# Optimization experiments

Measured on AMD Instinct MI355X. Metric: run time of the kernel, lower is better.

## Reference

```python
import jax, jax.numpy as jnp
import numpy as np


def conv1d_same(x, w, b):
    # x:[B,C,W], w:[O,I,K] -> [B,O,W] (stride 1, SAME padding, k=11,p=5)
    y = jax.lax.conv_general_dilated(x, w, (1,), 'SAME',
                                     dimension_numbers=('NCH', 'OIH', 'NCH'))
    return y + b[None, :, None]


def maxpool8(x):
    B, C, W = x.shape
    return x.reshape(B, C, W // 8, 8).max(axis=-1)


def encoder(x, p):
    back1 = jax.nn.relu(conv1d_same(x, p['e_c1_w'], p['e_c1_b']))   # [B,64,1280]
    h = maxpool8(back1)                                              # [B,64,160]
    back2 = jax.nn.relu(conv1d_same(h, p['e_c2_w'], p['e_c2_b']))   # [B,128,160]
    h = maxpool8(back2)                                              # [B,128,20]
    h = h.reshape(h.shape[0], -1)                                    # [B,2560]
    h = jax.nn.relu(h @ p['e_f1_w'].T + p['e_f1_b'])
    fea = jax.nn.sigmoid(h @ p['e_f2_w'].T + p['e_f2_b'])            # [B,64]
    return back1, back2, fea


def decoder(fea, back1, back2, p):
    h = jax.nn.relu(fea @ p['d_f1_w'].T + p['d_f1_b'])
    h = jax.nn.relu(h @ p['d_f2_w'].T + p['d_f2_b'])                 # [B,2560]
    h = h.reshape(h.shape[0], 128, 20)
    h = jnp.repeat(h, 8, axis=-1)                                    # nearest upsample -> 160
    h = jax.nn.relu(conv1d_same(jnp.concatenate([h, back2], 1), p['d_c2_w'], p['d_c2_b']))
    h = jnp.repeat(h, 8, axis=-1)                                    # -> 1280
    h = jax.nn.relu(conv1d_same(jnp.concatenate([h, back1], 1), p['d_c1_w'], p['d_c1_b']))
    return h                                                         # [B,2,1280]


def pairwise_kl(fea_s, fea_t, lab_s, lab_t, L):
    # Group rows by label. jnp.argsort is stable, so within each label the
    # original row order is preserved, exactly like torch boolean-mask gather.
    # Equal per-label counts are assumed (required by F.kl_div shape match).
    gs = fea_s[jnp.argsort(lab_s)].reshape(L, -1, fea_s.shape[-1])
    gt = fea_t[jnp.argsort(lab_t)].reshape(L, -1, fea_t.shape[-1])
    T = jnp.concatenate([gs, gt], axis=1)          # [L, M, D]
    logT = jnp.log(T)
    M = T.shape[1] * T.shape[2]
    # kl_div(t_i.log(), t_j) with reduction='mean' = mean(t_j*(log t_j - log t_i))
    A = jnp.sum(T * logT, axis=(1, 2)) / M         # [L]: mean(t_j log t_j)
    C = jnp.einsum('imd,jmd->ij', logT, T) / M     # C[i,j] = mean(t_j log t_i)
    kl = (L - 1) * A.sum() - (C.sum() - jnp.trace(C))  # sum over i != j
    return (kl / (L * L / 2.0))[None]              # shape [1] like torch.zeros(1)


def setup_inputs() -> dict:
    key = jax.random.key(0)
    ks = jax.random.split(key, 12)
    B, L, W = 256, 8, 1280

    def w(k, shape, fan_in):
        return (jax.random.normal(k, shape, jnp.float32) / np.sqrt(fan_in)).astype(jnp.float32)

    return {
        'x_source': jax.random.normal(ks[0], (B, 2, W), jnp.float32),
        'x_target': jax.random.normal(ks[1], (B, 2, W), jnp.float32),
        'x_s_label': jnp.arange(B, dtype=jnp.int32) % L,  # balanced labels
        'x_t_label': jnp.arange(B, dtype=jnp.int32) % L,
        'label_all': L,
        'e_c1_w': w(ks[2], (64, 2, 11), 2 * 11),    'e_c1_b': jnp.zeros(64, jnp.float32),
        'e_c2_w': w(ks[3], (128, 64, 11), 64 * 11), 'e_c2_b': jnp.zeros(128, jnp.float32),
        'e_f1_w': w(ks[4], (512, 2560), 2560),      'e_f1_b': jnp.zeros(512, jnp.float32),
        'e_f2_w': w(ks[5], (64, 512), 512),         'e_f2_b': jnp.zeros(64, jnp.float32),
        'd_f1_w': w(ks[6], (256, 64), 64),          'd_f1_b': jnp.zeros(256, jnp.float32),
        'd_f2_w': w(ks[7], (2560, 256), 256),       'd_f2_b': jnp.zeros(2560, jnp.float32),
        'd_c2_w': w(ks[8], (64, 256, 11), 256 * 11),'d_c2_b': jnp.zeros(64, jnp.float32),
        'd_c1_w': w(ks[9], (2, 128, 11), 128 * 11), 'd_c1_b': jnp.zeros(2, jnp.float32),
    }


def reference(x_source, x_target, x_s_label, x_t_label, label_all,
              e_c1_w, e_c1_b, e_c2_w, e_c2_b, e_f1_w, e_f1_b, e_f2_w, e_f2_b,
              d_f1_w, d_f1_b, d_f2_w, d_f2_b, d_c2_w, d_c2_b, d_c1_w, d_c1_b):
    p = {'e_c1_w': e_c1_w, 'e_c1_b': e_c1_b, 'e_c2_w': e_c2_w, 'e_c2_b': e_c2_b,
         'e_f1_w': e_f1_w, 'e_f1_b': e_f1_b, 'e_f2_w': e_f2_w, 'e_f2_b': e_f2_b,
         'd_f1_w': d_f1_w, 'd_f1_b': d_f1_b, 'd_f2_w': d_f2_w, 'd_f2_b': d_f2_b,
         'd_c2_w': d_c2_w, 'd_c2_b': d_c2_b, 'd_c1_w': d_c1_w, 'd_c1_b': d_c1_b}
    back1_s, back2_s, fea_s = encoder(x_source, p)
    back1_t, back2_t, fea_t = encoder(x_target, p)
    out_s = decoder(fea_s, back1_t, back2_t, p)
    out_t = decoder(fea_t, back1_s, back2_s, p)
    kl = pairwise_kl(fea_s, fea_t, x_s_label, x_t_label, label_all)
    return out_s, out_t, kl
```

## Files before the change

### kernel.cpp

```cpp
#include <hip/hip_runtime.h>
#include <hip/hip_bf16.h>
#include <math.h>

#define BB   256
#define LLc  8
#define DDc  64
#define GSc  32

typedef __attribute__((ext_vector_type(8))) short short8;
typedef __attribute__((ext_vector_type(4))) float f32x4;
typedef unsigned short u16;

__device__ inline float b2f(u16 h) { return __uint_as_float(((unsigned)h) << 16); }
__device__ inline u16 f2b(float f) {
  unsigned u = __float_as_uint(f);
  return (u16)((u + 0x7fffu + ((u >> 16) & 1u)) >> 16);
}

#define PRE_W2P   90112
#define PRE_WD2P  270336
#define PRE_WD1P  292864
#define PRE_EF1   1603584
#define PRE_DF2   2258944
#define PRE_UPT   2521088
#define PRE_B2T   3569664
#define PRE_W1P   3571712
#define PRE_B1T   4096000
#define PRE_D2T   4161536
__global__ __launch_bounds__(256) void prep_k(const float* __restrict__ ec2w, const float* __restrict__ dc2w,
                       const float* __restrict__ dc1w, const float* __restrict__ ef1w,
                       const float* __restrict__ df2w, const float* __restrict__ ec1w,
                       u16* __restrict__ W2p, u16* __restrict__ Wd2p, u16* __restrict__ Wd1p,
                       u16* __restrict__ ef1wbf, u16* __restrict__ df2wbf, u16* __restrict__ W1p,
                       u16* __restrict__ upT_s, u16* __restrict__ upT_t,
                       u16* __restrict__ b2T_s, u16* __restrict__ b2T_t,
                       u16* __restrict__ b1T_s, u16* __restrict__ b1T_t,
                       u16* __restrict__ d2T_s, u16* __restrict__ d2T_t) {
  int idx = blockIdx.x * 256 + threadIdx.x;
  if (idx < PRE_W2P) {
    int k = idx / 8192, oc = (idx / 64) % 128, ic = idx % 64;
    W2p[idx] = f2b(ec2w[(oc * 64 + ic) * 11 + k]);
  } else if (idx < PRE_WD2P) {
    int j = idx - PRE_W2P;
    int k = j / 16384, oc = (j / 256) % 64, icc = j % 256;
    Wd2p[j] = f2b(dc2w[(oc * 256 + icc) * 11 + k]);
  } else if (idx < PRE_WD1P) {
    int j = idx - PRE_WD2P;
    int k = j / 2048, rem = j % 2048;
    int chunk = rem / 512, oc = (rem / 32) % 16, c = rem % 32;
    Wd1p[j] = (oc < 2) ? f2b(dc1w[((size_t)oc * 128 + chunk * 32 + c) * 11 + k]) : 0;
  } else if (idx < PRE_EF1) {
    int j = idx - PRE_WD1P;
    ef1wbf[j] = f2b(ef1w[j]);
  } else if (idx < PRE_DF2) {
    int j = idx - PRE_EF1;
    df2wbf[j] = f2b(df2w[j]);
  } else if (idx < PRE_UPT) {
    int j = idx - PRE_DF2;
    int ic = j % 128, r4 = (j / 128) % 4, b = (j / 512) % 256, side = j / 131072;
    int row = (r4 == 0) ? 0 : (20 + r4);
    (side ? upT_t : upT_s)[((size_t)b * 24 + row) * 128 + ic] = 0;
  } else if (idx < PRE_B2T) {
    int j = idx - PRE_UPT;
    int ic = j % 128, pr = (j / 128) % 16, b = (j / 2048) % 256, side = j / 524288;
    int row = (pr < 8) ? pr : pr + 160;
    (side ? b2T_t : b2T_s)[((size_t)b * 176 + row) * 128 + ic] = 0;
  } else if (idx < PRE_W1P) {
    int j = idx - PRE_B2T;
    int oc = j >> 5, kk = j & 31, ic = kk >> 4, k = kk & 15;
    W1p[j] = (k < 11) ? f2b(ec1w[oc * 22 + ic * 11 + k]) : 0;
  } else if (idx < PRE_B1T) {
    int j = idx - PRE_W1P;
    int ic = j % 64, pr = (j / 64) % 16, b = (j / 1024) % 256, side = j / 262144;
    int row = (pr < 5) ? pr : 1280 + pr;
    (side ? b1T_t : b1T_s)[((size_t)b * 1296 + row) * 64 + ic] = 0;
  } else if (idx < PRE_D2T) {
    int j = idx - PRE_B1T;
    int ic = j % 64, pr = (j / 64) & 1, b = (j / 128) % 256, side = j / 32768;
    int row = pr ? 161 : 0;
    (side ? d2T_t : d2T_s)[((size_t)b * 162 + row) * 64 + ic] = 0;
  }
}

__global__ __launch_bounds__(256) void im2col1_k(const float* __restrict__ x_s, const float* __restrict__ x_t,
                          u16* __restrict__ xcol_s, u16* __restrict__ xcol_t) {
  int bk = blockIdx.x;
  int side = bk >= 320;
  int idx = (bk - (side ? 320 : 0)) * 256 + threadIdx.x;
  int wg = idx % 160, ic = (idx / 160) & 1, b = idx / 320;
  int w0 = wg * 8;
  const float* xb = (side ? x_t : x_s) + (size_t)(b * 2 + ic) * 1280;
  u16* xcol = side ? xcol_t : xcol_s;
  u16 win[18];
#pragma unroll
  for (int j = 0; j < 18; j++) {
    int p = w0 - 5 + j;
    win[j] = (p >= 0 && p < 1280) ? f2b(xb[p]) : 0;
  }
#pragma unroll
  for (int r = 0; r < 8; r++) {
    uint4 s0, s1;
    s0.x = (unsigned)win[r + 0] | ((unsigned)win[r + 1] << 16);
    s0.y = (unsigned)win[r + 2] | ((unsigned)win[r + 3] << 16);
    s0.z = (unsigned)win[r + 4] | ((unsigned)win[r + 5] << 16);
    s0.w = (unsigned)win[r + 6] | ((unsigned)win[r + 7] << 16);
    s1.x = (unsigned)win[r + 8] | ((unsigned)win[r + 9] << 16);
    s1.y = (unsigned)win[r + 10];
    s1.z = 0; s1.w = 0;
    u16* dst = xcol + ((size_t)(b * 1280 + w0 + r) * 32 + ic * 16);
    *(uint4*)dst = s0;
    *(uint4*)(dst + 8) = s1;
  }
}

__global__ __launch_bounds__(256) void conv1_mfma(const u16* __restrict__ xcol_s, const u16* __restrict__ xcol_t,
                           const u16* __restrict__ W1p, const float* __restrict__ bias,
                           u16* __restrict__ b1T_s, u16* __restrict__ b1T_t) {
  int blk = blockIdx.x;
  int side = blk >> 10;
  int r = blk & 1023;
  int b = r >> 2, wq = r & 3;
  const u16* xcol = side ? xcol_t : xcol_s;
  u16* back1T = side ? b1T_t : b1T_s;
  int tid = threadIdx.x, wid = tid >> 6, l = tid & 63;
  int l15 = l & 15, lq = l >> 4;
  int oc0 = wid * 16;
  int w0 = wq * 320;
  short8 a = *(const short8*)(W1p + (oc0 + l15) * 32 + lq * 8);
  f32x4 zero = {0.f, 0.f, 0.f, 0.f};
  f32x4 acc[20];
#pragma unroll
  for (int j = 0; j < 20; j++) acc[j] = zero;
  const u16* xb = xcol + (size_t)b * 1280 * 32;
#pragma unroll
  for (int nf = 0; nf < 20; nf++) {
    int w = w0 + nf * 16 + l15;
    short8 bf = *(const short8*)(xb + (size_t)w * 32 + lq * 8);
    acc[nf] = __builtin_amdgcn_mfma_f32_16x16x32_bf16(a, bf, acc[nf], 0, 0, 0);
  }
  int ocb = oc0 + lq * 4;
  float b0 = bias[ocb], b1 = bias[ocb + 1], b2 = bias[ocb + 2], b3 = bias[ocb + 3];
#pragma unroll
  for (int nf = 0; nf < 20; nf++) {
    int w = w0 + nf * 16 + l15;
    uint2 st;
    st.x = (unsigned)f2b(fmaxf(acc[nf][0] + b0, 0.f)) | ((unsigned)f2b(fmaxf(acc[nf][1] + b1, 0.f)) << 16);
    st.y = (unsigned)f2b(fmaxf(acc[nf][2] + b2, 0.f)) | ((unsigned)f2b(fmaxf(acc[nf][3] + b3, 0.f)) << 16);
    *(uint2*)(back1T + ((size_t)b * 1296 + w + 5) * 64 + ocb) = st;
  }
}

__global__ __launch_bounds__(256) void pool1T_k(const u16* __restrict__ b1T_s, const u16* __restrict__ b1T_t,
                         u16* __restrict__ p1T_s, u16* __restrict__ p1T_t) {
  int bk = blockIdx.x;
  int side = bk >= 11264;
  int idx = (bk - (side ? 11264 : 0)) * 256 + threadIdx.x;
  int ic = idx % 64, row = (idx / 64) % 176, b = idx / 11264;
  const u16* back1T = side ? b1T_t : b1T_s;
  u16 val = 0;
  if (row >= 8 && row < 168) {
    const u16* pp = back1T + ((size_t)b * 1296 + (row - 8) * 8 + 5) * 64 + ic;
    float m = b2f(pp[0]);
#pragma unroll
    for (int j = 1; j < 8; j++) m = fmaxf(m, b2f(pp[j * 64]));
    val = f2b(m);
  }
  (side ? p1T_t : p1T_s)[idx] = val;
}

__global__ __launch_bounds__(256) void conv2_split(const u16* __restrict__ p1T_s, const u16* __restrict__ p1T_t,
                            const u16* __restrict__ W2p, const float* __restrict__ bias,
                            u16* __restrict__ b2T_s, u16* __restrict__ b2T_t) {
  __shared__ u16 smem[90 * 72];
  int blk = blockIdx.x;
  int side = blk >> 10;
  int r = blk & 1023;
  int b = r >> 2, wh = (r >> 1) & 1, oh = r & 1;
  const u16* p1T = side ? p1T_t : p1T_s;
  u16* back2T = side ? b2T_t : b2T_s;
  int tid = threadIdx.x, wid = tid >> 6, l = tid & 63;
  int l15 = l & 15, lq = l >> 4;
  int oc0 = oh * 64 + wid * 16;
  int w0 = wh * 80;
  const u16* pb = p1T + (size_t)b * 176 * 64;
  for (int i = tid; i < 720; i += 256) {
    int row = i >> 3, seg = i & 7;
    *(uint4*)(&smem[row * 72 + seg * 8]) = *(const uint4*)(pb + ((size_t)(w0 + 3 + row)) * 64 + seg * 8);
  }
  __syncthreads();
  f32x4 zero = {0.f, 0.f, 0.f, 0.f};
  f32x4 acc[5];
#pragma unroll
  for (int j = 0; j < 5; j++) acc[j] = zero;
  for (int k = 0; k < 11; k++) {
    for (int ic0 = 0; ic0 < 64; ic0 += 32) {
      short8 a = *(const short8*)(W2p + ((k * 128 + oc0 + l15) * 64 + ic0 + lq * 8));
      short8 bf[5];
#pragma unroll
      for (int nf = 0; nf < 5; nf++)
        bf[nf] = *(const short8*)(&smem[(nf * 16 + l15 + k) * 72 + ic0 + lq * 8]);
#pragma unroll
      for (int nf = 0; nf < 5; nf++)
        acc[nf] = __builtin_amdgcn_mfma_f32_16x16x32_bf16(a, bf[nf], acc[nf], 0, 0, 0);
    }
  }
  int ocb = oc0 + lq * 4;
  float b0 = bias[ocb], b1 = bias[ocb + 1], b2 = bias[ocb + 2], b3 = bias[ocb + 3];
#pragma unroll
  for (int nf = 0; nf < 5; nf++) {
    int w = w0 + nf * 16 + l15;
    f32x4 v = acc[nf];
    uint2 st;
    st.x = (unsigned)f2b(fmaxf(v[0] + b0, 0.f)) | ((unsigned)f2b(fmaxf(v[1] + b1, 0.f)) << 16);
    st.y = (unsigned)f2b(fmaxf(v[2] + b2, 0.f)) | ((unsigned)f2b(fmaxf(v[3] + b3, 0.f)) << 16);
    *(uint2*)(back2T + ((size_t)(b * 176 + 8 + w) * 128 + ocb)) = st;
  }
}

__global__ __launch_bounds__(256) void pool2_k(const u16* __restrict__ b2T_s, const u16* __restrict__ b2T_t,
                        u16* __restrict__ p2bf_s, u16* __restrict__ p2bf_t) {
  int bk = blockIdx.x;
  int side = bk >= 2560;
  int idx = (bk - (side ? 2560 : 0)) * 256 + threadIdx.x;
  int wo = idx % 20, oc = (idx / 20) % 128, b = idx / 2560;
  const u16* b2T = side ? b2T_t : b2T_s;
  float m = -1e30f;
#pragma unroll
  for (int j = 0; j < 8; j++)
    m = fmaxf(m, b2f(b2T[((size_t)b * 176 + 8 + wo * 8 + j) * 128 + oc]));
  (side ? p2bf_t : p2bf_s)[idx] = f2b(m);
}

__global__ __launch_bounds__(256) void ef1_split(const u16* __restrict__ A_s, const u16* __restrict__ A_t,
                          const u16* __restrict__ Bw, float* __restrict__ pbuf) {
  int blk = blockIdx.x;
  int side = blk >> 8;
  int r = blk & 255;
  int kc = r >> 5;
  int q = r & 31;
  int n0 = (q & 7) * 64;
  int tid = threadIdx.x, wid = tid >> 6, l = tid & 63;
  int l15 = l & 15, lq = l >> 4;
  int m0 = (q >> 3) * 64 + wid * 16;
  const u16* A = side ? A_t : A_s;
  f32x4 zero = {0.f, 0.f, 0.f, 0.f};
  f32x4 acc[4];
#pragma unroll
  for (int j = 0; j < 4; j++) acc[j] = zero;
  int kbase = kc * 320;
  for (int k0 = kbase; k0 < kbase + 320; k0 += 32) {
    short8 af = *(const short8*)(A + ((size_t)(m0 + l15) * 2560 + k0 + lq * 8));
    short8 bf[4];
#pragma unroll
    for (int nf = 0; nf < 4; nf++)
      bf[nf] = *(const short8*)(Bw + ((size_t)(n0 + nf * 16 + l15) * 2560 + k0 + lq * 8));
#pragma unroll
    for (int nf = 0; nf < 4; nf++)
      acc[nf] = __builtin_amdgcn_mfma_f32_16x16x32_bf16(af, bf[nf], acc[nf], 0, 0, 0);
  }
  int bb = m0 + lq * 4;
  float* pb = pbuf + (size_t)(side * 8 + kc) * 131072;
#pragma unroll
  for (int nf = 0; nf < 4; nf++) {
    int oc = n0 + nf * 16 + l15;
#pragma unroll
    for (int rr = 0; rr < 4; rr++)
      pb[(size_t)(bb + rr) * 512 + oc] = acc[nf][rr];
  }
}

__global__ __launch_bounds__(256) void ef1_red(const float* __restrict__ pbuf, const float* __restrict__ bias,
                        float* __restrict__ ef1_s, float* __restrict__ ef1_t) {
  int e = blockIdx.x * 256 + threadIdx.x;
  int side = e >> 17;
  int j = e & 131071;
  const float* pb = pbuf + (size_t)side * 8 * 131072;
  float s = 0.f;
#pragma unroll
  for (int kc = 0; kc < 8; kc++) s += pb[(size_t)kc * 131072 + j];
  s += bias[j & 511];
  (side ? ef1_t : ef1_s)[j] = fmaxf(s, 0.f);
}

__global__ __launch_bounds__(256) void ef2df1_k(const float* __restrict__ ef1_s, const float* __restrict__ ef1_t,
                         const float* __restrict__ ef2w, const float* __restrict__ ef2b,
                         const float* __restrict__ df1w, const float* __restrict__ df1b,
                         float* __restrict__ fea_s, float* __restrict__ fea_t,
                         u16* __restrict__ df1bf_s, u16* __restrict__ df1bf_t) {
  __shared__ float row[512];
  __shared__ float part[256];
  __shared__ float fea_sh[64];
  int side = blockIdx.x >> 8;
  int b = blockIdx.x & 255;
  const float* ef1 = side ? ef1_t : ef1_s;
  float* fea = side ? fea_t : fea_s;
  u16* df1bf = side ? df1bf_t : df1bf_s;
  int tid = threadIdx.x;
  row[tid] = ef1[(size_t)b * 512 + tid];
  row[tid + 256] = ef1[(size_t)b * 512 + tid + 256];
  __syncthreads();
  {
    int o = tid & 63, q = tid >> 6;
    const float4* wr = (const float4*)(ef2w + (size_t)o * 512 + q * 128);
    float s = 0.f;
    int base = q * 128;
#pragma unroll
    for (int i = 0; i < 32; i++) {
      float4 wv = wr[i];
      s += row[base + 4 * i] * wv.x + row[base + 4 * i + 1] * wv.y +
           row[base + 4 * i + 2] * wv.z + row[base + 4 * i + 3] * wv.w;
    }
    part[q * 64 + o] = s;
  }
  __syncthreads();
  if (tid < 64) {
    float v = part[tid] + part[64 + tid] + part[128 + tid] + part[192 + tid] + ef2b[tid];
    float sg = 1.f / (1.f + expf(-v));
    fea_sh[tid] = sg;
    fea[(size_t)b * 64 + tid] = sg;
  }
  __syncthreads();
  {
    const float4* wr = (const float4*)(df1w + (size_t)tid * 64);
    float s = 0.f;
#pragma unroll
    for (int i = 0; i < 16; i++) {
      float4 wv = wr[i];
      s += fea_sh[4 * i] * wv.x + fea_sh[4 * i + 1] * wv.y +
           fea_sh[4 * i + 2] * wv.z + fea_sh[4 * i + 3] * wv.w;
    }
    df1bf[(size_t)b * 256 + tid] = f2b(fmaxf(s + df1b[tid], 0.f));
  }
}

__global__ __launch_bounds__(256) void df2_gemm(const u16* __restrict__ A_s, const u16* __restrict__ A_t,
                         const u16* __restrict__ Bw, const float* __restrict__ bias,
                         u16* __restrict__ upT_s, u16* __restrict__ upT_t) {
  int blk = blockIdx.x;
  int side = blk >= 40;
  int n0 = (blk - (side ? 40 : 0)) * 64;
  const u16* A = side ? A_t : A_s;
  u16* upT = side ? upT_t : upT_s;
  int tid = threadIdx.x, wid = tid >> 6, l = tid & 63;
  int l15 = l & 15, lq = l >> 4;
  int m0 = wid * 64;
  f32x4 zero = {0.f, 0.f, 0.f, 0.f};
  f32x4 acc[4][4];
#pragma unroll
  for (int i = 0; i < 4; i++)
#pragma unroll
    for (int j = 0; j < 4; j++) acc[i][j] = zero;
  for (int k0 = 0; k0 < 256; k0 += 32) {
    short8 af[4], bf[4];
#pragma unroll
    for (int mf = 0; mf < 4; mf++)
      af[mf] = *(const short8*)(A + ((size_t)(m0 + mf * 16 + l15) * 256 + k0 + lq * 8));
#pragma unroll
    for (int nf = 0; nf < 4; nf++)
      bf[nf] = *(const short8*)(Bw + ((size_t)(n0 + nf * 16 + l15) * 256 + k0 + lq * 8));
#pragma unroll
    for (int mf = 0; mf < 4; mf++)
#pragma unroll
      for (int nf = 0; nf < 4; nf++)
        acc[mf][nf] = __builtin_amdgcn_mfma_f32_16x16x32_bf16(af[mf], bf[nf], acc[mf][nf], 0, 0, 0);
  }
#pragma unroll
  for (int nf = 0; nf < 4; nf++) {
    int o = n0 + nf * 16 + l15;
    float bi = bias[o];
    int ch = o / 20, t = o - ch * 20;
#pragma unroll
    for (int mf = 0; mf < 4; mf++) {
      int bb = m0 + mf * 16 + lq * 4;
#pragma unroll
      for (int r = 0; r < 4; r++)
        upT[((size_t)(bb + r) * 24 + 1 + t) * 128 + ch] = f2b(fmaxf(acc[mf][nf][r] + bi, 0.f));
    }
  }
}

__global__ __launch_bounds__(256) void convd2_split(const u16* __restrict__ upT_s, const u16* __restrict__ upT_t,
                             const u16* __restrict__ b2T_s, const u16* __restrict__ b2T_t,
                             const u16* __restrict__ Wd2p, float* __restrict__ part) {
  __shared__ u16 smem[90 * 136];
  int blk = blockIdx.x;
  int side = blk >> 10;
  int r = blk & 1023;
  int b = r >> 2, wh = (r >> 1) & 1, khalf = r & 1;
  const u16* upT   = side ? upT_t : upT_s;
  const u16* skipT = side ? b2T_s : b2T_t;
  int tid = threadIdx.x, wid = tid >> 6, l = tid & 63;
  int l15 = l & 15, lq = l >> 4;
  int oc0 = wid * 16;
  int w0 = wh * 80;
  const u16* sb = skipT + (size_t)b * 176 * 128;
  for (int i = tid; i < 1440; i += 256) {
    int row = i >> 4, seg = i & 15;
    *(uint4*)(&smem[row * 136 + seg * 8]) = *(const uint4*)(sb + ((size_t)(w0 + 3 + row)) * 128 + seg * 8);
  }
  __syncthreads();
  f32x4 zero = {0.f, 0.f, 0.f, 0.f};
  f32x4 acc[5];
#pragma unroll
  for (int j = 0; j < 5; j++) acc[j] = zero;
  const u16* ub = upT + (size_t)b * 24 * 128;
  int kbeg = khalf ? 6 : 0, kend = khalf ? 11 : 6;
  for (int k = kbeg; k < kend; k++) {
    for (int ic0 = 0; ic0 < 128; ic0 += 32) {
      short8 a = *(const short8*)(Wd2p + ((k * 64 + oc0 + l15) * 256 + ic0 + lq * 8));
#pragma unroll
      for (int nf = 0; nf < 5; nf++) {
        int w = w0 + nf * 16 + l15;
        int rr = (w + k + 3) >> 3;
        short8 bf = *(const short8*)(ub + (rr * 128 + ic0 + lq * 8));
        acc[nf] = __builtin_amdgcn_mfma_f32_16x16x32_bf16(a, bf, acc[nf], 0, 0, 0);
      }
    }
    for (int ic0 = 0; ic0 < 128; ic0 += 32) {
      short8 a = *(const short8*)(Wd2p + ((k * 64 + oc0 + l15) * 256 + 128 + ic0 + lq * 8));
#pragma unroll
      for (int nf = 0; nf < 5; nf++) {
        short8 bf = *(const short8*)(&smem[(nf * 16 + l15 + k) * 136 + ic0 + lq * 8]);
        acc[nf] = __builtin_amdgcn_mfma_f32_16x16x32_bf16(a, bf, acc[nf], 0, 0, 0);
      }
    }
  }
  float* pp = part + (((size_t)(side * 2 + khalf) * 256 + b) * 160) * 64;
  int ocb = oc0 + lq * 4;
#pragma unroll
  for (int nf = 0; nf < 5; nf++) {
    int w = w0 + nf * 16 + l15;
    *(f32x4*)(pp + (size_t)w * 64 + ocb) = acc[nf];
  }
}

__global__ __launch_bounds__(256) void convd2_red(const float* __restrict__ part, const float* __restrict__ bias,
                           u16* __restrict__ d2T_s, u16* __restrict__ d2T_t) {
  int idx = blockIdx.x * 256 + threadIdx.x;
  int oc4 = (idx & 15) * 4;
  int w = (idx >> 4) % 160;
  int rb = (idx >> 4) / 160;
  int b = rb & 255;
  int side = rb >> 8;
  const float* p0 = part + (((size_t)(side * 2 + 0) * 256 + b) * 160 + w) * 64 + oc4;
  const float* p1 = part + (((size_t)(side * 2 + 1) * 256 + b) * 160 + w) * 64 + oc4;
  float4 a = *(const float4*)p0;
  float4 c = *(const float4*)p1;
  float b0 = bias[oc4], b1 = bias[oc4 + 1], b2 = bias[oc4 + 2], b3 = bias[oc4 + 3];
  uint2 st;
  st.x = (unsigned)f2b(fmaxf(a.x + c.x + b0, 0.f)) | ((unsigned)f2b(fmaxf(a.y + c.y + b1, 0.f)) << 16);
  st.y = (unsigned)f2b(fmaxf(a.z + c.z + b2, 0.f)) | ((unsigned)f2b(fmaxf(a.w + c.w + b3, 0.f)) << 16);
  u16* dst = side ? d2T_t : d2T_s;
  *(uint2*)(dst + ((size_t)b * 162 + w + 1) * 64 + oc4) = st;
}

__global__ __launch_bounds__(256) void convd1_mfma(const u16* __restrict__ d2T_s, const u16* __restrict__ d2T_t,
                            const u16* __restrict__ b1T_s, const u16* __restrict__ b1T_t,
                            const u16* __restrict__ Wd1p, const float* __restrict__ bias,
                            float* __restrict__ out_s, float* __restrict__ out_t) {
  __shared__ u16 smem[330 * 72];
  int blk = blockIdx.x;
  int side = blk >> 10;
  int r = blk & 1023;
  int b = r >> 2, q = r & 3;
  const u16* dc2T   = side ? d2T_t : d2T_s;
  const u16* back1T = side ? b1T_s : b1T_t;
  float* out = side ? out_t : out_s;
  int tid = threadIdx.x, wid = tid >> 6, l = tid & 63;
  int l15 = l & 15, lq = l >> 4;
  int base = q * 320;
  int wloc0 = wid * 80;
  const u16* sb = back1T + (size_t)b * 1296 * 64;
  for (int i = tid; i < 2640; i += 256) {
    int row = i >> 3, seg = i & 7;
    *(uint4*)(&smem[row * 72 + seg * 8]) = *(const uint4*)(sb + ((size_t)(base + row)) * 64 + seg * 8);
  }
  __syncthreads();
  f32x4 zero = {0.f, 0.f, 0.f, 0.f};
  f32x4 acc[5];
#pragma unroll
  for (int j = 0; j < 5; j++) acc[j] = zero;
  const u16* ub = dc2T + (size_t)b * 162 * 64;
  for (int k = 0; k < 11; k++) {
#pragma unroll
    for (int ch = 0; ch < 2; ch++) {
      short8 wf = *(const short8*)(Wd1p + ((k * 4 + ch) * 16 + l15) * 32 + lq * 8);
#pragma unroll
      for (int nf = 0; nf < 5; nf++) {
        int w = base + wloc0 + nf * 16 + l15;
        int rr = (w + k + 3) >> 3;
        short8 af = *(const short8*)(ub + (rr * 64 + ch * 32 + lq * 8));
        acc[nf] = __builtin_amdgcn_mfma_f32_16x16x32_bf16(af, wf, acc[nf], 0, 0, 0);
      }
    }
#pragma unroll
    for (int ch = 0; ch < 2; ch++) {
      short8 wf = *(const short8*)(Wd1p + ((k * 4 + 2 + ch) * 16 + l15) * 32 + lq * 8);
#pragma unroll
      for (int nf = 0; nf < 5; nf++) {
        int lrow = wloc0 + nf * 16 + l15 + k;
        short8 af = *(const short8*)(&smem[lrow * 72 + ch * 32 + lq * 8]);
        acc[nf] = __builtin_amdgcn_mfma_f32_16x16x32_bf16(af, wf, acc[nf], 0, 0, 0);
      }
    }
  }
  if (l15 < 2) {
    float bi = bias[l15];
    float* ob = out + ((size_t)b * 2 + l15) * 1280;
#pragma unroll
    for (int nf = 0; nf < 5; nf++) {
      int wbase = base + wloc0 + nf * 16 + lq * 4;
      float4 v;
      v.x = fmaxf(acc[nf][0] + bi, 0.f);
      v.y = fmaxf(acc[nf][1] + bi, 0.f);
      v.z = fmaxf(acc[nf][2] + bi, 0.f);
      v.w = fmaxf(acc[nf][3] + bi, 0.f);
      *(float4*)(ob + wbase) = v;
    }
  }
}

__global__ void kl_sort_k(const int* __restrict__ lab_s, const int* __restrict__ lab_t,
                          int* __restrict__ srt) {
  int t = threadIdx.x;
  {
    int lab = lab_s[t];
    int pos = 0;
    for (int b = 0; b < BB; b++) {
      int lb = lab_s[b];
      pos += (lb < lab) + ((b < t) && (lb == lab));
    }
    srt[pos] = t;
  }
  {
    int lab = lab_t[t];
    int pos = 0;
    for (int b = 0; b < BB; b++) {
      int lb = lab_t[b];
      pos += (lb < lab) + ((b < t) && (lb == lab));
    }
    srt[256 + pos] = t;
  }
}

__global__ void kl_build_k(const float* __restrict__ fea_s, const float* __restrict__ fea_t,
                           const int* __restrict__ srt,
                           float* __restrict__ T, float* __restrict__ logT) {
  int idx = blockIdx.x * 256 + threadIdx.x;
#pragma unroll
  for (int r = 0; r < 4; r++) {
    int e = idx + r * 8192;
    int d = e & 63;
    int m = (e >> 6) & 63;
    int l = e >> 12;
    float v;
    if (m < GSc) v = fea_s[srt[l * GSc + m] * DDc + d];
    else         v = fea_t[srt[256 + l * GSc + (m - GSc)] * DDc + d];
    T[e]    = v;
    logT[e] = logf(v);
  }
}

__global__ void kl_pairs_k(const float* __restrict__ T, const float* __restrict__ logT,
                           float* __restrict__ C) {
  int blk = blockIdx.x;
  int i = blk >> 3, j = blk & 7;
  int t = threadIdx.x;
  __shared__ float wsum[4];
  const float* li = logT + i * 4096;
  const float* tj = T + j * 4096;
  float s = 0.f;
  for (int e = t; e < 4096; e += 256) s += li[e] * tj[e];
  for (int off = 32; off > 0; off >>= 1) s += __shfl_down(s, off, 64);
  if ((t & 63) == 0) wsum[t >> 6] = s;
  __syncthreads();
  if (t == 0) C[blk] = wsum[0] + wsum[1] + wsum[2] + wsum[3];
}

__global__ void kl_final_k(const float* __restrict__ C, float* __restrict__ out) {
  int t = threadIdx.x;
  float c = C[t];
  float tr = ((t >> 3) == (t & 7)) ? c : 0.f;
  for (int off = 32; off > 0; off >>= 1) {
    c  += __shfl_down(c, off, 64);
    tr += __shfl_down(tr, off, 64);
  }
  if (t == 0) out[0] = (LLc * tr - c) / 4096.f / (LLc * LLc / 2.0f);
}

extern "C" void kernel_launch(void* const* d_in, const int* in_sizes, int n_in,
                              void* d_out, int out_size, void* d_ws, size_t ws_size,
                              hipStream_t stream) {
  const float* x_s  = (const float*)d_in[0];
  const float* x_t  = (const float*)d_in[1];
  const int* lab_s  = (const int*)d_in[2];
  const int* lab_t  = (const int*)d_in[3];
  const float* ec1w = (const float*)d_in[5];  const float* ec1b = (const float*)d_in[6];
  const float* ec2w = (const float*)d_in[7];  const float* ec2b = (const float*)d_in[8];
  const float* ef1w = (const float*)d_in[9];  const float* ef1b = (const float*)d_in[10];
  const float* ef2w = (const float*)d_in[11]; const float* ef2b = (const float*)d_in[12];
  const float* df1w = (const float*)d_in[13]; const float* df1b = (const float*)d_in[14];
  const float* df2w = (const float*)d_in[15]; const float* df2b = (const float*)d_in[16];
  const float* dc2w = (const float*)d_in[17]; const float* dc2b = (const float*)d_in[18];
  const float* dc1w = (const float*)d_in[19]; const float* dc1b = (const float*)d_in[20];

  char* p = (char*)d_ws;
  auto alloc = [&](size_t bytes) -> char* {
    char* r = p;
    p += (bytes + 255) & ~(size_t)255;
    return r;
  };
  u16*   b1T_s   = (u16*)alloc((size_t)BB * 1296 * 64 * 2);
  u16*   b1T_t   = (u16*)alloc((size_t)BB * 1296 * 64 * 2);
  u16*   xcol_s  = (u16*)alloc((size_t)BB * 1280 * 32 * 2);
  u16*   xcol_t  = (u16*)alloc((size_t)BB * 1280 * 32 * 2);
  u16*   p1T_s   = (u16*)alloc((size_t)BB * 176 * 64 * 2);
  u16*   p1T_t   = (u16*)alloc((size_t)BB * 176 * 64 * 2);
  u16*   b2T_s   = (u16*)alloc((size_t)BB * 176 * 128 * 2);
  u16*   b2T_t   = (u16*)alloc((size_t)BB * 176 * 128 * 2);
  u16*   upT_s   = (u16*)alloc((size_t)BB * 24 * 128 * 2);
  u16*   upT_t   = (u16*)alloc((size_t)BB * 24 * 128 * 2);
  u16*   p2bf_s  = (u16*)alloc((size_t)BB * 2560 * 2);
  u16*   p2bf_t  = (u16*)alloc((size_t)BB * 2560 * 2);
  float* ef1_s   = (float*)alloc((size_t)BB * 512 * 4);
  float* ef1_t   = (float*)alloc((size_t)BB * 512 * 4);
  float* fea_s   = (float*)alloc((size_t)BB * 64 * 4);
  float* fea_t   = (float*)alloc((size_t)BB * 64 * 4);
  u16*   df1bf_s = (u16*)alloc((size_t)BB * 256 * 2);
  u16*   df1bf_t = (u16*)alloc((size_t)BB * 256 * 2);
  u16*   d2T_s   = (u16*)alloc((size_t)BB * 162 * 64 * 2);
  u16*   d2T_t   = (u16*)alloc((size_t)BB * 162 * 64 * 2);
  u16*   W2p     = (u16*)alloc(90112 * 2);
  u16*   Wd2p    = (u16*)alloc(180224 * 2);
  u16*   Wd1p    = (u16*)alloc(22528 * 2);
  u16*   ef1wbf  = (u16*)alloc((size_t)1310720 * 2);
  u16*   df2wbf  = (u16*)alloc((size_t)655360 * 2);
  u16*   W1p     = (u16*)alloc(2048 * 2);
  float* Tbuf    = (float*)alloc((size_t)32768 * 4);
  float* logTbuf = (float*)alloc((size_t)32768 * 4);
  int*   srt     = (int*)alloc(512 * 4);
  float* Cbuf    = (float*)alloc(64 * 4);
  float* pbuf    = (float*)xcol_s;
  float* part    = (float*)xcol_t;

  float* out_s  = (float*)d_out;
  float* out_t  = out_s + (size_t)BB * 2 * 1280;
  float* out_kl = out_s + (size_t)2 * BB * 2 * 1280;

  dim3 blk(256);

  prep_k<<<dim3(16256), blk, 0, stream>>>(ec2w, dc2w, dc1w, ef1w, df2w, ec1w,
                                          W2p, Wd2p, Wd1p, ef1wbf, df2wbf, W1p,
                                          upT_s, upT_t, b2T_s, b2T_t,
                                          b1T_s, b1T_t, d2T_s, d2T_t);

  im2col1_k<<<dim3(640), blk, 0, stream>>>(x_s, x_t, xcol_s, xcol_t);
  conv1_mfma<<<dim3(2048), blk, 0, stream>>>(xcol_s, xcol_t, W1p, ec1b, b1T_s, b1T_t);
  pool1T_k<<<dim3(22528), blk, 0, stream>>>(b1T_s, b1T_t, p1T_s, p1T_t);
  conv2_split<<<dim3(2048), blk, 0, stream>>>(p1T_s, p1T_t, W2p, ec2b, b2T_s, b2T_t);
  pool2_k<<<dim3(5120), blk, 0, stream>>>(b2T_s, b2T_t, p2bf_s, p2bf_t);
  ef1_split<<<dim3(512), blk, 0, stream>>>(p2bf_s, p2bf_t, ef1wbf, pbuf);
  ef1_red<<<dim3(1024), blk, 0, stream>>>(pbuf, ef1b, ef1_s, ef1_t);
  ef2df1_k<<<dim3(512), blk, 0, stream>>>(ef1_s, ef1_t, ef2w, ef2b, df1w, df1b,
                                          fea_s, fea_t, df1bf_s, df1bf_t);

  df2_gemm<<<dim3(80), blk, 0, stream>>>(df1bf_s, df1bf_t, df2wbf, df2b, upT_s, upT_t);
  convd2_split<<<dim3(2048), blk, 0, stream>>>(upT_s, upT_t, b2T_s, b2T_t, Wd2p, part);
  convd2_red<<<dim3(5120), blk, 0, stream>>>(part, dc2b, d2T_s, d2T_t);
  convd1_mfma<<<dim3(2048), blk, 0, stream>>>(d2T_s, d2T_t, b1T_s, b1T_t, Wd1p, dc1b, out_s, out_t);

  kl_sort_k<<<dim3(1), blk, 0, stream>>>(lab_s, lab_t, srt);
  kl_build_k<<<dim3(32), blk, 0, stream>>>(fea_s, fea_t, srt, Tbuf, logTbuf);
  kl_pairs_k<<<dim3(64), blk, 0, stream>>>(Tbuf, logTbuf, Cbuf);
  kl_final_k<<<dim3(1), dim3(64), 0, stream>>>(Cbuf, out_kl);
}
```

Before: 489.7 us.

## Swizzle LDS rows in conv kernels and merge convd2 split-K with its reduction

Applies an XOR-like rotation swizzle to the shared-memory row layout in conv2, convd2 and convd1, so MFMA operand reads from LDS avoid bank conflicts caused by the 72/136-element row stride. Separately, it drops the two-way K split in the decoder conv2 together with its fp32 partial buffer and reduction kernel. One kernel now runs all 11 taps and applies bias, ReLU and the bf16 store directly. This removes a launch and the partial-sum round trip through global memory, but halves the block count for that stage, which lowers parallelism.

```diff
diff --git a/kernel.cpp b/kernel.cpp
--- a/kernel.cpp
+++ b/kernel.cpp
@@ -185,7 +185,8 @@
   const u16* pb = p1T + (size_t)b * 176 * 64;
   for (int i = tid; i < 720; i += 256) {
     int row = i >> 3, seg = i & 7;
-    *(uint4*)(&smem[row * 72 + seg * 8]) = *(const uint4*)(pb + ((size_t)(w0 + 3 + row)) * 64 + seg * 8);
+    int sl = (seg + 2 * row) & 7;
+    *(uint4*)(&smem[row * 72 + sl * 8]) = *(const uint4*)(pb + ((size_t)(w0 + 3 + row)) * 64 + seg * 8);
   }
   __syncthreads();
   f32x4 zero = {0.f, 0.f, 0.f, 0.f};
@@ -197,8 +198,11 @@
       short8 a = *(const short8*)(W2p + ((k * 128 + oc0 + l15) * 64 + ic0 + lq * 8));
       short8 bf[5];
 #pragma unroll
-      for (int nf = 0; nf < 5; nf++)
-        bf[nf] = *(const short8*)(&smem[(nf * 16 + l15 + k) * 72 + ic0 + lq * 8]);
+      for (int nf = 0; nf < 5; nf++) {
+        int lrow = nf * 16 + l15 + k;
+        int sl = ((ic0 >> 3) + lq + 2 * lrow) & 7;
+        bf[nf] = *(const short8*)(&smem[lrow * 72 + (sl << 3)]);
+      }
 #pragma unroll
       for (int nf = 0; nf < 5; nf++)
         acc[nf] = __builtin_amdgcn_mfma_f32_16x16x32_bf16(a, bf[nf], acc[nf], 0, 0, 0);
@@ -379,16 +383,18 @@
   }
 }
 
-__global__ __launch_bounds__(256) void convd2_split(const u16* __restrict__ upT_s, const u16* __restrict__ upT_t,
-                             const u16* __restrict__ b2T_s, const u16* __restrict__ b2T_t,
-                             const u16* __restrict__ Wd2p, float* __restrict__ part) {
+__global__ __launch_bounds__(256) void convd2_mfma(const u16* __restrict__ upT_s, const u16* __restrict__ upT_t,
+                            const u16* __restrict__ b2T_s, const u16* __restrict__ b2T_t,
+                            const u16* __restrict__ Wd2p, const float* __restrict__ bias,
+                            u16* __restrict__ d2T_s, u16* __restrict__ d2T_t) {
   __shared__ u16 smem[90 * 136];
   int blk = blockIdx.x;
-  int side = blk >> 10;
-  int r = blk & 1023;
-  int b = r >> 2, wh = (r >> 1) & 1, khalf = r & 1;
+  int side = blk >> 9;
+  int r = blk & 511;
+  int b = r >> 1, wh = r & 1;
   const u16* upT   = side ? upT_t : upT_s;
   const u16* skipT = side ? b2T_s : b2T_t;
+  u16* dc2T = side ? d2T_t : d2T_s;
   int tid = threadIdx.x, wid = tid >> 6, l = tid & 63;
   int l15 = l & 15, lq = l >> 4;
   int oc0 = wid * 16;
@@ -396,7 +402,8 @@
   const u16* sb = skipT + (size_t)b * 176 * 128;
   for (int i = tid; i < 1440; i += 256) {
     int row = i >> 4, seg = i & 15;
-    *(uint4*)(&smem[row * 136 + seg * 8]) = *(const uint4*)(sb + ((size_t)(w0 + 3 + row)) * 128 + seg * 8);
+    int sl = (seg + 2 * row) & 15;
+    *(uint4*)(&smem[row * 136 + sl * 8]) = *(const uint4*)(sb + ((size_t)(w0 + 3 + row)) * 128 + seg * 8);
   }
   __syncthreads();
   f32x4 zero = {0.f, 0.f, 0.f, 0.f};
@@ -404,8 +411,7 @@
 #pragma unroll
   for (int j = 0; j < 5; j++) acc[j] = zero;
   const u16* ub = upT + (size_t)b * 24 * 128;
-  int kbeg = khalf ? 6 : 0, kend = khalf ? 11 : 6;
-  for (int k = kbeg; k < kend; k++) {
+  for (int k = 0; k < 11; k++) {
     for (int ic0 = 0; ic0 < 128; ic0 += 32) {
       short8 a = *(const short8*)(Wd2p + ((k * 64 + oc0 + l15) * 256 + ic0 + lq * 8));
 #pragma unroll
@@ -420,38 +426,23 @@
       short8 a = *(const short8*)(Wd2p + ((k * 64 + oc0 + l15) * 256 + 128 + ic0 + lq * 8));
 #pragma unroll
       for (int nf = 0; nf < 5; nf++) {
-        short8 bf = *(const short8*)(&smem[(nf * 16 + l15 + k) * 136 + ic0 + lq * 8]);
+        int lrow = nf * 16 + l15 + k;
+        int sl = ((ic0 >> 3) + lq + 2 * lrow) & 15;
+        short8 bf = *(const short8*)(&smem[lrow * 136 + (sl << 3)]);
         acc[nf] = __builtin_amdgcn_mfma_f32_16x16x32_bf16(a, bf, acc[nf], 0, 0, 0);
       }
     }
   }
-  float* pp = part + (((size_t)(side * 2 + khalf) * 256 + b) * 160) * 64;
   int ocb = oc0 + lq * 4;
+  float bb0 = bias[ocb], bb1 = bias[ocb + 1], bb2 = bias[ocb + 2], bb3 = bias[ocb + 3];
 #pragma unroll
   for (int nf = 0; nf < 5; nf++) {
     int w = w0 + nf * 16 + l15;
-    *(f32x4*)(pp + (size_t)w * 64 + ocb) = acc[nf];
-  }
-}
-
-__global__ __launch_bounds__(256) void convd2_red(const float* __restrict__ part, const float* __restrict__ bias,
-                           u16* __restrict__ d2T_s, u16* __restrict__ d2T_t) {
-  int idx = blockIdx.x * 256 + threadIdx.x;
-  int oc4 = (idx & 15) * 4;
-  int w = (idx >> 4) % 160;
-  int rb = (idx >> 4) / 160;
-  int b = rb & 255;
-  int side = rb >> 8;
-  const float* p0 = part + (((size_t)(side * 2 + 0) * 256 + b) * 160 + w) * 64 + oc4;
-  const float* p1 = part + (((size_t)(side * 2 + 1) * 256 + b) * 160 + w) * 64 + oc4;
-  float4 a = *(const float4*)p0;
-  float4 c = *(const float4*)p1;
-  float b0 = bias[oc4], b1 = bias[oc4 + 1], b2 = bias[oc4 + 2], b3 = bias[oc4 + 3];
-  uint2 st;
-  st.x = (unsigned)f2b(fmaxf(a.x + c.x + b0, 0.f)) | ((unsigned)f2b(fmaxf(a.y + c.y + b1, 0.f)) << 16);
-  st.y = (unsigned)f2b(fmaxf(a.z + c.z + b2, 0.f)) | ((unsigned)f2b(fmaxf(a.w + c.w + b3, 0.f)) << 16);
-  u16* dst = side ? d2T_t : d2T_s;
-  *(uint2*)(dst + ((size_t)b * 162 + w + 1) * 64 + oc4) = st;
+    uint2 st;
+    st.x = (unsigned)f2b(fmaxf(acc[nf][0] + bb0, 0.f)) | ((unsigned)f2b(fmaxf(acc[nf][1] + bb1, 0.f)) << 16);
+    st.y = (unsigned)f2b(fmaxf(acc[nf][2] + bb2, 0.f)) | ((unsigned)f2b(fmaxf(acc[nf][3] + bb3, 0.f)) << 16);
+    *(uint2*)(dc2T + ((size_t)b * 162 + w + 1) * 64 + ocb) = st;
+  }
 }
 
 __global__ __launch_bounds__(256) void convd1_mfma(const u16* __restrict__ d2T_s, const u16* __restrict__ d2T_t,
@@ -473,7 +464,8 @@
   const u16* sb = back1T + (size_t)b * 1296 * 64;
   for (int i = tid; i < 2640; i += 256) {
     int row = i >> 3, seg = i & 7;
-    *(uint4*)(&smem[row * 72 + seg * 8]) = *(const uint4*)(sb + ((size_t)(base + row)) * 64 + seg * 8);
+    int sl = (seg + 2 * row) & 7;
+    *(uint4*)(&smem[row * 72 + sl * 8]) = *(const uint4*)(sb + ((size_t)(base + row)) * 64 + seg * 8);
   }
   __syncthreads();
   f32x4 zero = {0.f, 0.f, 0.f, 0.f};
@@ -499,7 +491,8 @@
 #pragma unroll
       for (int nf = 0; nf < 5; nf++) {
         int lrow = wloc0 + nf * 16 + l15 + k;
-        short8 af = *(const short8*)(&smem[lrow * 72 + ch * 32 + lq * 8]);
+        int sl = (ch * 4 + lq + 2 * lrow) & 7;
+        short8 af = *(const short8*)(&smem[lrow * 72 + (sl << 3)]);
         acc[nf] = __builtin_amdgcn_mfma_f32_16x16x32_bf16(af, wf, acc[nf], 0, 0, 0);
       }
     }
@@ -641,7 +634,6 @@
   int*   srt     = (int*)alloc(512 * 4);
   float* Cbuf    = (float*)alloc(64 * 4);
   float* pbuf    = (float*)xcol_s;
-  float* part    = (float*)xcol_t;
 
   float* out_s  = (float*)d_out;
   float* out_t  = out_s + (size_t)BB * 2 * 1280;
@@ -665,8 +657,7 @@
                                           fea_s, fea_t, df1bf_s, df1bf_t);
 
   df2_gemm<<<dim3(80), blk, 0, stream>>>(df1bf_s, df1bf_t, df2wbf, df2b, upT_s, upT_t);
-  convd2_split<<<dim3(2048), blk, 0, stream>>>(upT_s, upT_t, b2T_s, b2T_t, Wd2p, part);
-  convd2_red<<<dim3(5120), blk, 0, stream>>>(part, dc2b, d2T_s, d2T_t);
+  convd2_mfma<<<dim3(1024), blk, 0, stream>>>(upT_s, upT_t, b2T_s, b2T_t, Wd2p, dc2b, d2T_s, d2T_t);
   convd1_mfma<<<dim3(2048), blk, 0, stream>>>(d2T_s, d2T_t, b1T_s, b1T_t, Wd1p, dc1b, out_s, out_t);
 
   kl_sort_k<<<dim3(1), blk, 0, stream>>>(lab_s, lab_t, srt);
```

New measurement: 470.0 us. 1.04x faster.
